# Performance work log

Measured on AMD Instinct MI355X. Metric: run time of the kernel, lower is better.

Reference implementation:

```python
import jax, jax.numpy as jnp
import numpy as np

B, E, H, L, V = 128, 1024, 1024, 2, 32001  # vocab = output_size + 1
PAD_IDX = 1000


def gru_cell(x, h, w_ih, w_hh, b_ih, b_hh):
    # PyTorch GRU cell math; gates ordered (r, z, n)
    gi = x @ w_ih.T + b_ih            # [B, 3H]
    gh = h @ w_hh.T + b_hh            # [B, 3H]
    i_r, i_z, i_n = jnp.split(gi, 3, axis=-1)
    h_r, h_z, h_n = jnp.split(gh, 3, axis=-1)
    r = jax.nn.sigmoid(i_r + h_r)
    z = jax.nn.sigmoid(i_z + h_z)
    n = jnp.tanh(i_n + r * h_n)
    return (1.0 - z) * n + z * h


def setup_inputs() -> dict:
    key = jax.random.key(0)
    ks = jax.random.split(key, 16)
    input_vector = jax.random.randint(ks[0], (B,), 0, V)
    hidden = jax.random.normal(ks[1], (L, B, H), dtype=jnp.float32)
    emb = jax.random.uniform(ks[2], (V, E), minval=-0.1, maxval=0.1, dtype=jnp.float32)
    emb = emb.at[PAD_IDX].set(0.0)  # padding_idx
    s = 1.0 / np.sqrt(H)
    def u(k, shape):
        return jax.random.uniform(k, shape, minval=-s, maxval=s, dtype=jnp.float32)
    w_ih0 = u(ks[3], (3 * H, E)); w_hh0 = u(ks[4], (3 * H, H))
    b_ih0 = u(ks[5], (3 * H,));  b_hh0 = u(ks[6], (3 * H,))
    w_ih1 = u(ks[7], (3 * H, H)); w_hh1 = u(ks[8], (3 * H, H))
    b_ih1 = u(ks[9], (3 * H,));  b_hh1 = u(ks[10], (3 * H,))
    w_out = jax.random.uniform(ks[11], (V, H), minval=-0.1, maxval=0.1, dtype=jnp.float32)
    b_out = jnp.zeros((V,), dtype=jnp.float32)
    return dict(input_vector=input_vector, hidden=hidden, emb=emb,
                w_ih0=w_ih0, w_hh0=w_hh0, b_ih0=b_ih0, b_hh0=b_hh0,
                w_ih1=w_ih1, w_hh1=w_hh1, b_ih1=b_ih1, b_hh1=b_hh1,
                w_out=w_out, b_out=b_out)


def reference(input_vector, hidden, emb, w_ih0, w_hh0, b_ih0, b_hh0,
              w_ih1, w_hh1, b_ih1, b_hh1, w_out, b_out):
    x = jax.nn.relu(emb[input_vector])          # [B, E] (seq_len=1 squeezed)
    h0 = gru_cell(x, hidden[0], w_ih0, w_hh0, b_ih0, b_hh0)   # [B, H]
    h1 = gru_cell(h0, hidden[1], w_ih1, w_hh1, b_ih1, b_hh1)  # [B, H]
    logits = h1 @ w_out.T + b_out               # [B, V]
    out = jax.nn.log_softmax(logits, axis=-1)   # [B, V]
    hidden_out = jnp.stack([h0, h1], axis=0)    # [L, B, H]
    return out, hidden_out
```

## Files before the change

### kernel.cpp

```cpp
#include <hip/hip_runtime.h>
#include <cmath>

#define BATCH 128
#define KDIM 1024
#define VOCAB 32001
#define G3 3072
#define GIP_STRIDE (BATCH * G3)

typedef __bf16 bf16_t;
typedef bf16_t bf16x8 __attribute__((ext_vector_type(8)));
typedef float f32x4 __attribute__((ext_vector_type(4)));

__device__ __forceinline__ void stage16(const void* g, void* lds) {
    __builtin_amdgcn_global_load_lds(
        (const __attribute__((address_space(1))) void*)g,
        (__attribute__((address_space(3))) void*)lds, 16, 0, 0);
}

template<bool BIAS>
__device__ __forceinline__ void gemm_core(
    const bf16_t* __restrict__ A, const float* __restrict__ W,
    const float* __restrict__ bias, float* __restrict__ C,
    int ldc, int Wrows, int n0, int kbeg, int kend)
{
    __shared__ bf16_t sA[128 * 64];
    __shared__ float  sB[64 * 64];
    const int t    = threadIdx.x;
    const int wave = t >> 6;
    const int lane = t & 63;
    const int l15  = lane & 15;
    const int quad = lane >> 4;
    const int wm   = wave & 1;
    const int wn   = wave >> 1;

    const bf16_t* aSrc[4]; int aDst[4];
#pragma unroll
    for (int r = 0; r < 4; ++r) {
        const int row = r * 32 + (t >> 3);
        const int sg  = t & 7;
        const int kg  = sg ^ (row & 7);
        aSrc[r] = A + (size_t)row * KDIM + kg * 8 + kbeg;
        aDst[r] = row * 128 + sg * 16;
    }
    const float* wSrc[4]; int wDst[4];
#pragma unroll
    for (int r = 0; r < 4; ++r) {
        const int row = r * 16 + (t >> 4);
        int wr = n0 + row; if (wr > Wrows - 1) wr = Wrows - 1;
        const int sg = t & 15;
        const int kg = sg ^ (row & 15);
        wSrc[r] = W + (size_t)wr * KDIM + kg * 4 + kbeg;
        wDst[r] = row * 256 + sg * 16;
    }

    f32x4 acc[4][2];
#pragma unroll
    for (int i = 0; i < 4; ++i)
#pragma unroll
        for (int j = 0; j < 2; ++j) acc[i][j] = f32x4{0.f, 0.f, 0.f, 0.f};

    for (int k0 = 0; k0 < kend - kbeg; k0 += 64) {
#pragma unroll
        for (int r = 0; r < 4; ++r) stage16(aSrc[r] + k0, (char*)sA + aDst[r]);
#pragma unroll
        for (int r = 0; r < 4; ++r) stage16(wSrc[r] + k0, (char*)sB + wDst[r]);
        __syncthreads();
#pragma unroll
        for (int s = 0; s < 2; ++s) {
            bf16x8 bfr[2];
#pragma unroll
            for (int j = 0; j < 2; ++j) {
                const int row = wn * 32 + j * 16 + l15;
                const int gu  = (s * 8 + 2 * quad) ^ (row & 15);
                const f32x4 u = *(const f32x4*)((const char*)sB + row * 256 + gu * 16);
                const f32x4 v = *(const f32x4*)((const char*)sB + row * 256 + (gu ^ 1) * 16);
                bf16x8 b;
                b[0] = (bf16_t)u[0]; b[1] = (bf16_t)u[1]; b[2] = (bf16_t)u[2]; b[3] = (bf16_t)u[3];
                b[4] = (bf16_t)v[0]; b[5] = (bf16_t)v[1]; b[6] = (bf16_t)v[2]; b[7] = (bf16_t)v[3];
                bfr[j] = b;
            }
#pragma unroll
            for (int i = 0; i < 4; ++i) {
                const int row  = wm * 64 + i * 16 + l15;
                const int phys = (s * 4 + quad) ^ (row & 7);
                const bf16x8 af = *(const bf16x8*)((const char*)sA + row * 128 + phys * 16);
#pragma unroll
                for (int j = 0; j < 2; ++j)
                    acc[i][j] = __builtin_amdgcn_mfma_f32_16x16x32_bf16(
                        af, bfr[j], acc[i][j], 0, 0, 0);
            }
        }
        __syncthreads();
    }

#pragma unroll
    for (int j = 0; j < 2; ++j) {
        const int col = n0 + wn * 32 + j * 16 + l15;
        if (col < Wrows) {
            const float bv = BIAS ? bias[col] : 0.f;
#pragma unroll
            for (int i = 0; i < 4; ++i)
#pragma unroll
                for (int r = 0; r < 4; ++r) {
                    const int row = wm * 64 + i * 16 + quad * 4 + r;
                    C[(size_t)row * ldc + col] = acc[i][j][r] + bv;
                }
        }
    }
}

__global__ __launch_bounds__(256, 4) void gemm_gru(
    const bf16_t* __restrict__ Ai, const float* __restrict__ wih,
    float* __restrict__ giP,
    const bf16_t* __restrict__ Ah, const float* __restrict__ whh,
    float* __restrict__ ghP)
{
    const int split = blockIdx.x;
    const int n0    = blockIdx.y * 64;
    const int kbeg  = split * 256;
    if (blockIdx.z == 0)
        gemm_core<false>(Ai, wih, nullptr, giP + (size_t)split * GIP_STRIDE,
                         G3, G3, n0, kbeg, kbeg + 256);
    else
        gemm_core<false>(Ah, whh, nullptr, ghP + (size_t)split * GIP_STRIDE,
                         G3, G3, n0, kbeg, kbeg + 256);
}

__global__ __launch_bounds__(256, 4) void gemm_vocab(
    const bf16_t* __restrict__ A, const float* __restrict__ W,
    const float* __restrict__ bias, float* __restrict__ C)
{
    gemm_core<true>(A, W, bias, C, VOCAB, VOCAB, blockIdx.x * 64, 0, KDIM);
}

__global__ __launch_bounds__(256) void prep_bf16(const int* __restrict__ idx,
                                                 const float* __restrict__ emb,
                                                 const float* __restrict__ hidden,
                                                 bf16_t* __restrict__ dst) {
    const int i = blockIdx.x * 256 + threadIdx.x;
    const int sec = i >> 15;
    const int j   = i & 32767;
    f32x4 v;
    if (sec == 0) {
        const int b = j >> 8, e4 = j & 255;
        v = ((const f32x4*)(emb + (size_t)idx[b] * KDIM))[e4];
#pragma unroll
        for (int k = 0; k < 4; ++k) v[k] = fmaxf(v[k], 0.f);
    } else {
        v = ((const f32x4*)(hidden + (size_t)(sec - 1) * (BATCH * KDIM)))[j];
    }
    bf16_t o[4];
#pragma unroll
    for (int k = 0; k < 4; ++k) o[k] = (bf16_t)v[k];
    *(uint64_t*)(dst + (size_t)i * 4) = *(const uint64_t*)o;
}

__device__ __forceinline__ f32x4 sum_splits(const float* p) {
    f32x4 s = *(const f32x4*)p;
    s += *(const f32x4*)(p + GIP_STRIDE);
    s += *(const f32x4*)(p + 2 * GIP_STRIDE);
    s += *(const f32x4*)(p + 3 * GIP_STRIDE);
    return s;
}

__global__ __launch_bounds__(256) void gru_gate(const float* __restrict__ giP,
                                                const float* __restrict__ ghP,
                                                const float* __restrict__ b_ih,
                                                const float* __restrict__ b_hh,
                                                const float* __restrict__ hprev,
                                                float* __restrict__ hout,
                                                bf16_t* __restrict__ hout_bf16) {
    const int i  = blockIdx.x * 256 + threadIdx.x;
    const int b  = i >> 8;
    const int j  = (i & 255) * 4;
    const size_t base = (size_t)b * G3 + j;

    f32x4 ir = sum_splits(giP + base),        hr = sum_splits(ghP + base);
    f32x4 iz = sum_splits(giP + base + 1024), hz = sum_splits(ghP + base + 1024);
    f32x4 in = sum_splits(giP + base + 2048), hn = sum_splits(ghP + base + 2048);
    const f32x4 bir = *(const f32x4*)(b_ih + j);
    const f32x4 biz = *(const f32x4*)(b_ih + j + 1024);
    const f32x4 bin = *(const f32x4*)(b_ih + j + 2048);
    const f32x4 bhr = *(const f32x4*)(b_hh + j);
    const f32x4 bhz = *(const f32x4*)(b_hh + j + 1024);
    const f32x4 bhn = *(const f32x4*)(b_hh + j + 2048);
    const f32x4 hp  = *(const f32x4*)(hprev + (size_t)b * KDIM + j);

    f32x4 o;
    bf16_t ob[4];
#pragma unroll
    for (int k = 0; k < 4; ++k) {
        const float r = 1.f / (1.f + __expf(-(ir[k] + bir[k] + hr[k] + bhr[k])));
        const float z = 1.f / (1.f + __expf(-(iz[k] + biz[k] + hz[k] + bhz[k])));
        const float a = in[k] + bin[k] + r * (hn[k] + bhn[k]);
        const float n = 1.f - 2.f / (__expf(2.f * a) + 1.f);
        o[k] = (1.f - z) * n + z * hp[k];
        ob[k] = (bf16_t)o[k];
    }
    *(f32x4*)(hout + (size_t)b * KDIM + j) = o;
    *(uint64_t*)(hout_bf16 + (size_t)b * KDIM + j) = *(const uint64_t*)ob;
}

__global__ __launch_bounds__(1024) void log_softmax_rows(float* __restrict__ out) {
    float* row = out + (size_t)blockIdx.x * VOCAB;
    const int t = threadIdx.x;
    __shared__ float sm[16], ss[16];

    float m = -3.4e38f, s = 0.f;
    for (int i = t; i < VOCAB; i += 1024) {
        const float v  = row[i];
        const float mn = fmaxf(m, v);
        s = s * __expf(m - mn) + __expf(v - mn);
        m = mn;
    }
#pragma unroll
    for (int o = 32; o; o >>= 1) {
        const float mo = __shfl_down(m, o);
        const float so = __shfl_down(s, o);
        const float mn = fmaxf(m, mo);
        s = s * __expf(m - mn) + so * __expf(mo - mn);
        m = mn;
    }
    if ((t & 63) == 0) { sm[t >> 6] = m; ss[t >> 6] = s; }
    __syncthreads();
    if (t == 0) {
        float M = sm[0], S = ss[0];
#pragma unroll
        for (int w = 1; w < 16; ++w) {
            const float mn = fmaxf(M, sm[w]);
            S = S * __expf(M - mn) + ss[w] * __expf(sm[w] - mn);
            M = mn;
        }
        sm[0] = M + __logf(S);
    }
    __syncthreads();
    const float L = sm[0];

    for (int i = t * 4; i + 3 < VOCAB; i += 4096) {
        f32x4 v = *(const f32x4*)(row + i);
        v[0] -= L; v[1] -= L; v[2] -= L; v[3] -= L;
        *(f32x4*)(row + i) = v;
    }
    if (t == 0) row[32000] -= L;
}

extern "C" void kernel_launch(void* const* d_in, const int* in_sizes, int n_in,
                              void* d_out, int out_size, void* d_ws, size_t ws_size,
                              hipStream_t stream) {
    const int*   ivec  = (const int*)  d_in[0];
    const float* hidden= (const float*)d_in[1];
    const float* emb   = (const float*)d_in[2];
    const float* w_ih0 = (const float*)d_in[3];
    const float* w_hh0 = (const float*)d_in[4];
    const float* b_ih0 = (const float*)d_in[5];
    const float* b_hh0 = (const float*)d_in[6];
    const float* w_ih1 = (const float*)d_in[7];
    const float* w_hh1 = (const float*)d_in[8];
    const float* b_ih1 = (const float*)d_in[9];
    const float* b_hh1 = (const float*)d_in[10];
    const float* w_out = (const float*)d_in[11];
    const float* b_out = (const float*)d_in[12];

    float* out = (float*)d_out;
    float* h0  = out + (size_t)BATCH * VOCAB;
    float* h1  = h0 + BATCH * KDIM;

    float*  ws   = (float*)d_ws;
    float*  giP  = ws;
    float*  ghP  = ws + 4 * (size_t)GIP_STRIDE;
    bf16_t* xb   = (bf16_t*)(ws + 8 * (size_t)GIP_STRIDE);
    bf16_t* hp0b = xb   + BATCH * KDIM;
    bf16_t* hp1b = hp0b + BATCH * KDIM;
    bf16_t* h0b  = hp1b + BATCH * KDIM;
    bf16_t* h1b  = h0b  + BATCH * KDIM;

    const float* hprev0 = hidden;
    const float* hprev1 = hidden + BATCH * KDIM;

    prep_bf16<<<384, 256, 0, stream>>>(ivec, emb, hidden, xb);

    gemm_gru<<<dim3(4, 48, 2), 256, 0, stream>>>(xb, w_ih0, giP, hp0b, w_hh0, ghP);
    gru_gate<<<128, 256, 0, stream>>>(giP, ghP, b_ih0, b_hh0, hprev0, h0, h0b);

    gemm_gru<<<dim3(4, 48, 2), 256, 0, stream>>>(h0b, w_ih1, giP, hp1b, w_hh1, ghP);
    gru_gate<<<128, 256, 0, stream>>>(giP, ghP, b_ih1, b_hh1, hprev1, h1, h1b);

    gemm_vocab<<<501, 256, 0, stream>>>(h1b, w_out, b_out, out);

    log_softmax_rows<<<128, 1024, 0, stream>>>(out);
}
```

Baseline: 336.6 us.

## Fuse softmax statistics into vocab GEMM epilogue and raise GRU split-K to 8

The vocab GEMM now computes per-row partial max/sum-exp for each 64-column tile in its epilogue and writes them to a stats buffer. A lighter softmax_final kernel merges those stats and subtracts the log-sum-exp over a 2D grid, so the extra full read pass over the logits goes away. The GRU GEMMs move from 4 to 8 K-splits for more parallelism, at the cost of more partial-sum traffic in the gate kernel. The vocab GEMM also doubles its K tile to 128 and drops to 2 blocks per CU, and the gate kernel now uses 128-thread blocks.

Result: no change. 338.0 us (+0.4%).

```diff
diff --git a/kernel.cpp b/kernel.cpp
--- a/kernel.cpp
+++ b/kernel.cpp
@@ -5,6 +5,7 @@
 #define KDIM 1024
 #define VOCAB 32001
 #define G3 3072
+#define NSPLIT 8
 #define GIP_STRIDE (BATCH * G3)
 
 typedef __bf16 bf16_t;
@@ -17,12 +18,25 @@
         (__attribute__((address_space(3))) void*)lds, 16, 0, 0);
 }
 
-template<bool BIAS>
-__device__ __forceinline__ void gemm_core(
-    const bf16_t* __restrict__ A, const float* __restrict__ W,
-    const float* __restrict__ bias, float* __restrict__ C,
-    int ldc, int Wrows, int n0, int kbeg, int kend)
+__device__ __forceinline__ void smerge(float& m, float& s, float mo, float so) {
+    const float mn = fmaxf(m, mo);
+    s = s * __expf(m - mn) + so * __expf(mo - mn);
+    m = mn;
+}
+
+__global__ __launch_bounds__(256, 4) void gemm_gru(
+    const bf16_t* __restrict__ Ai, const float* __restrict__ wih,
+    float* __restrict__ giP,
+    const bf16_t* __restrict__ Ah, const float* __restrict__ whh,
+    float* __restrict__ ghP)
 {
+    const int split = blockIdx.x;
+    const int n0    = blockIdx.y * 64;
+    const int kbeg  = split * 128;
+    const bf16_t* A; const float* W; float* C;
+    if (blockIdx.z == 0) { A = Ai; W = wih; C = giP + (size_t)split * GIP_STRIDE; }
+    else                 { A = Ah; W = whh; C = ghP + (size_t)split * GIP_STRIDE; }
+
     __shared__ bf16_t sA[128 * 64];
     __shared__ float  sB[64 * 64];
     const int t    = threadIdx.x;
@@ -38,18 +52,15 @@
     for (int r = 0; r < 4; ++r) {
         const int row = r * 32 + (t >> 3);
         const int sg  = t & 7;
-        const int kg  = sg ^ (row & 7);
-        aSrc[r] = A + (size_t)row * KDIM + kg * 8 + kbeg;
+        aSrc[r] = A + (size_t)row * KDIM + (sg ^ (row & 7)) * 8 + kbeg;
         aDst[r] = row * 128 + sg * 16;
     }
     const float* wSrc[4]; int wDst[4];
 #pragma unroll
     for (int r = 0; r < 4; ++r) {
         const int row = r * 16 + (t >> 4);
-        int wr = n0 + row; if (wr > Wrows - 1) wr = Wrows - 1;
-        const int sg = t & 15;
-        const int kg = sg ^ (row & 15);
-        wSrc[r] = W + (size_t)wr * KDIM + kg * 4 + kbeg;
+        const int sg  = t & 15;
+        wSrc[r] = W + (size_t)(n0 + row) * KDIM + (sg ^ (row & 15)) * 4 + kbeg;
         wDst[r] = row * 256 + sg * 16;
     }
 
@@ -59,7 +70,8 @@
 #pragma unroll
         for (int j = 0; j < 2; ++j) acc[i][j] = f32x4{0.f, 0.f, 0.f, 0.f};
 
-    for (int k0 = 0; k0 < kend - kbeg; k0 += 64) {
+#pragma unroll
+    for (int k0 = 0; k0 < 128; k0 += 64) {
 #pragma unroll
         for (int r = 0; r < 4; ++r) stage16(aSrc[r] + k0, (char*)sA + aDst[r]);
 #pragma unroll
@@ -96,41 +108,131 @@
 #pragma unroll
     for (int j = 0; j < 2; ++j) {
         const int col = n0 + wn * 32 + j * 16 + l15;
-        if (col < Wrows) {
-            const float bv = BIAS ? bias[col] : 0.f;
-#pragma unroll
-            for (int i = 0; i < 4; ++i)
-#pragma unroll
-                for (int r = 0; r < 4; ++r) {
-                    const int row = wm * 64 + i * 16 + quad * 4 + r;
-                    C[(size_t)row * ldc + col] = acc[i][j][r] + bv;
-                }
+#pragma unroll
+        for (int i = 0; i < 4; ++i)
+#pragma unroll
+            for (int r = 0; r < 4; ++r) {
+                const int row = wm * 64 + i * 16 + quad * 4 + r;
+                C[(size_t)row * G3 + col] = acc[i][j][r];
+            }
+    }
+}
+
+__global__ __launch_bounds__(256, 2) void gemm_vocab(
+    const bf16_t* __restrict__ A, const float* __restrict__ W,
+    const float* __restrict__ bias, float* __restrict__ C,
+    float2* __restrict__ stats)
+{
+    __shared__ bf16_t sA[128 * 128];
+    __shared__ float  sB[64 * 128];
+    const int t    = threadIdx.x;
+    const int wave = t >> 6;
+    const int lane = t & 63;
+    const int l15  = lane & 15;
+    const int quad = lane >> 4;
+    const int wm   = wave & 1;
+    const int wn   = wave >> 1;
+    const int n0   = blockIdx.x * 64;
+
+    const bf16_t* aSrc[8]; int aDst[8];
+#pragma unroll
+    for (int r = 0; r < 8; ++r) {
+        const int row = r * 16 + (t >> 4);
+        const int sg  = t & 15;
+        aSrc[r] = A + (size_t)row * KDIM + (sg ^ (row & 7)) * 8;
+        aDst[r] = row * 256 + sg * 16;
+    }
+    const float* wSrc[8]; int wDst[8];
+#pragma unroll
+    for (int r = 0; r < 8; ++r) {
+        const int row = r * 8 + (t >> 5);
+        int wr = n0 + row; if (wr > VOCAB - 1) wr = VOCAB - 1;
+        const int sg = t & 31;
+        wSrc[r] = W + (size_t)wr * KDIM + (sg ^ (row & 7)) * 4;
+        wDst[r] = row * 512 + sg * 16;
+    }
+
+    f32x4 acc[4][2];
+#pragma unroll
+    for (int i = 0; i < 4; ++i)
+#pragma unroll
+        for (int j = 0; j < 2; ++j) acc[i][j] = f32x4{0.f, 0.f, 0.f, 0.f};
+
+    for (int k0 = 0; k0 < KDIM; k0 += 128) {
+#pragma unroll
+        for (int r = 0; r < 8; ++r) stage16(aSrc[r] + k0, (char*)sA + aDst[r]);
+#pragma unroll
+        for (int r = 0; r < 8; ++r) stage16(wSrc[r] + k0, (char*)sB + wDst[r]);
+        __syncthreads();
+#pragma unroll
+        for (int s = 0; s < 4; ++s) {
+            bf16x8 bfr[2];
+#pragma unroll
+            for (int j = 0; j < 2; ++j) {
+                const int row = wn * 32 + j * 16 + l15;
+                const int g0  = s * 8 + quad * 2;
+                const int p0  = g0 ^ (row & 7);
+                const int p1  = (g0 + 1) ^ (row & 7);
+                const f32x4 u = *(const f32x4*)((const char*)sB + row * 512 + p0 * 16);
+                const f32x4 v = *(const f32x4*)((const char*)sB + row * 512 + p1 * 16);
+                bf16x8 b;
+                b[0] = (bf16_t)u[0]; b[1] = (bf16_t)u[1]; b[2] = (bf16_t)u[2]; b[3] = (bf16_t)u[3];
+                b[4] = (bf16_t)v[0]; b[5] = (bf16_t)v[1]; b[6] = (bf16_t)v[2]; b[7] = (bf16_t)v[3];
+                bfr[j] = b;
+            }
+#pragma unroll
+            for (int i = 0; i < 4; ++i) {
+                const int row  = wm * 64 + i * 16 + l15;
+                const int phys = (s * 4 + quad) ^ (row & 7);
+                const bf16x8 af = *(const bf16x8*)((const char*)sA + row * 256 + phys * 16);
+#pragma unroll
+                for (int j = 0; j < 2; ++j)
+                    acc[i][j] = __builtin_amdgcn_mfma_f32_16x16x32_bf16(
+                        af, bfr[j], acc[i][j], 0, 0, 0);
+            }
         }
-    }
-}
-
-__global__ __launch_bounds__(256, 4) void gemm_gru(
-    const bf16_t* __restrict__ Ai, const float* __restrict__ wih,
-    float* __restrict__ giP,
-    const bf16_t* __restrict__ Ah, const float* __restrict__ whh,
-    float* __restrict__ ghP)
-{
-    const int split = blockIdx.x;
-    const int n0    = blockIdx.y * 64;
-    const int kbeg  = split * 256;
-    if (blockIdx.z == 0)
-        gemm_core<false>(Ai, wih, nullptr, giP + (size_t)split * GIP_STRIDE,
-                         G3, G3, n0, kbeg, kbeg + 256);
-    else
-        gemm_core<false>(Ah, whh, nullptr, ghP + (size_t)split * GIP_STRIDE,
-                         G3, G3, n0, kbeg, kbeg + 256);
-}
-
-__global__ __launch_bounds__(256, 4) void gemm_vocab(
-    const bf16_t* __restrict__ A, const float* __restrict__ W,
-    const float* __restrict__ bias, float* __restrict__ C)
-{
-    gemm_core<true>(A, W, bias, C, VOCAB, VOCAB, blockIdx.x * 64, 0, KDIM);
+        __syncthreads();
+    }
+
+    int   col[2]; float bv[2];
+#pragma unroll
+    for (int j = 0; j < 2; ++j) {
+        col[j] = n0 + wn * 32 + j * 16 + l15;
+        bv[j]  = (col[j] < VOCAB) ? bias[col[j]] : 0.f;
+    }
+    float rm[4][4], rs[4][4];
+#pragma unroll
+    for (int i = 0; i < 4; ++i)
+#pragma unroll
+        for (int r = 0; r < 4; ++r) {
+            const int grow = wm * 64 + i * 16 + quad * 4 + r;
+            float v0 = acc[i][0][r] + bv[0];
+            float v1 = acc[i][1][r] + bv[1];
+            if (col[0] < VOCAB) C[(size_t)grow * VOCAB + col[0]] = v0; else v0 = -3.4e38f;
+            if (col[1] < VOCAB) C[(size_t)grow * VOCAB + col[1]] = v1; else v1 = -3.4e38f;
+            const float mm = fmaxf(v0, v1);
+            rm[i][r] = mm;
+            rs[i][r] = __expf(v0 - mm) + __expf(v1 - mm);
+#pragma unroll
+            for (int o = 1; o < 16; o <<= 1)
+                smerge(rm[i][r], rs[i][r], __shfl_xor(rm[i][r], o), __shfl_xor(rs[i][r], o));
+        }
+
+    __syncthreads();
+    float2* sst = (float2*)sA;
+#pragma unroll
+    for (int i = 0; i < 4; ++i)
+#pragma unroll
+        for (int r = 0; r < 4; ++r)
+            if (l15 == 0)
+                sst[wn * 128 + wm * 64 + i * 16 + quad * 4 + r] =
+                    make_float2(rm[i][r], rs[i][r]);
+    __syncthreads();
+    if (t < 128) {
+        float2 a = sst[t], b = sst[128 + t];
+        smerge(a.x, a.y, b.x, b.y);
+        stats[(size_t)t * 512 + blockIdx.x] = a;
+    }
 }
 
 __global__ __launch_bounds__(256) void prep_bf16(const int* __restrict__ idx,
@@ -157,20 +259,19 @@
 
 __device__ __forceinline__ f32x4 sum_splits(const float* p) {
     f32x4 s = *(const f32x4*)p;
-    s += *(const f32x4*)(p + GIP_STRIDE);
-    s += *(const f32x4*)(p + 2 * GIP_STRIDE);
-    s += *(const f32x4*)(p + 3 * GIP_STRIDE);
+#pragma unroll
+    for (int k = 1; k < NSPLIT; ++k) s += *(const f32x4*)(p + (size_t)k * GIP_STRIDE);
     return s;
 }
 
-__global__ __launch_bounds__(256) void gru_gate(const float* __restrict__ giP,
+__global__ __launch_bounds__(128) void gru_gate(const float* __restrict__ giP,
                                                 const float* __restrict__ ghP,
                                                 const float* __restrict__ b_ih,
                                                 const float* __restrict__ b_hh,
                                                 const float* __restrict__ hprev,
                                                 float* __restrict__ hout,
                                                 bf16_t* __restrict__ hout_bf16) {
-    const int i  = blockIdx.x * 256 + threadIdx.x;
+    const int i  = blockIdx.x * 128 + threadIdx.x;
     const int b  = i >> 8;
     const int j  = (i & 255) * 4;
     const size_t base = (size_t)b * G3 + j;
@@ -201,47 +302,40 @@
     *(uint64_t*)(hout_bf16 + (size_t)b * KDIM + j) = *(const uint64_t*)ob;
 }
 
-__global__ __launch_bounds__(1024) void log_softmax_rows(float* __restrict__ out) {
-    float* row = out + (size_t)blockIdx.x * VOCAB;
-    const int t = threadIdx.x;
-    __shared__ float sm[16], ss[16];
-
+__global__ __launch_bounds__(256) void softmax_final(float* __restrict__ out,
+                                                     const float2* __restrict__ stats) {
+    const int row = blockIdx.x, chunk = blockIdx.y, t = threadIdx.x;
     float m = -3.4e38f, s = 0.f;
-    for (int i = t; i < VOCAB; i += 1024) {
-        const float v  = row[i];
-        const float mn = fmaxf(m, v);
-        s = s * __expf(m - mn) + __expf(v - mn);
-        m = mn;
+    for (int k = t; k < 501; k += 256) {
+        const float2 p = stats[(size_t)row * 512 + k];
+        smerge(m, s, p.x, p.y);
     }
 #pragma unroll
     for (int o = 32; o; o >>= 1) {
         const float mo = __shfl_down(m, o);
         const float so = __shfl_down(s, o);
-        const float mn = fmaxf(m, mo);
-        s = s * __expf(m - mn) + so * __expf(mo - mn);
-        m = mn;
-    }
-    if ((t & 63) == 0) { sm[t >> 6] = m; ss[t >> 6] = s; }
+        smerge(m, s, mo, so);
+    }
+    __shared__ float sm[4], ssu[4], sL;
+    if ((t & 63) == 0) { sm[t >> 6] = m; ssu[t >> 6] = s; }
     __syncthreads();
     if (t == 0) {
-        float M = sm[0], S = ss[0];
-#pragma unroll
-        for (int w = 1; w < 16; ++w) {
-            const float mn = fmaxf(M, sm[w]);
-            S = S * __expf(M - mn) + ss[w] * __expf(sm[w] - mn);
-            M = mn;
-        }
-        sm[0] = M + __logf(S);
+        float M = sm[0], S = ssu[0];
+#pragma unroll
+        for (int w = 1; w < 4; ++w) smerge(M, S, sm[w], ssu[w]);
+        sL = M + __logf(S);
     }
     __syncthreads();
-    const float L = sm[0];
-
-    for (int i = t * 4; i + 3 < VOCAB; i += 4096) {
-        f32x4 v = *(const f32x4*)(row + i);
+    const float L = sL;
+
+    float* rowp = out + (size_t)row * VOCAB;
+    const int g = chunk * 256 + t;
+    for (int i = g * 4; i + 3 < VOCAB; i += 4096) {
+        f32x4 v = *(const f32x4*)(rowp + i);
         v[0] -= L; v[1] -= L; v[2] -= L; v[3] -= L;
-        *(f32x4*)(row + i) = v;
-    }
-    if (t == 0) row[32000] -= L;
+        *(f32x4*)(rowp + i) = v;
+    }
+    if (g == 0) rowp[32000] -= L;
 }
 
 extern "C" void kernel_launch(void* const* d_in, const int* in_sizes, int n_in,
@@ -265,27 +359,28 @@
     float* h0  = out + (size_t)BATCH * VOCAB;
     float* h1  = h0 + BATCH * KDIM;
 
-    float*  ws   = (float*)d_ws;
-    float*  giP  = ws;
-    float*  ghP  = ws + 4 * (size_t)GIP_STRIDE;
-    bf16_t* xb   = (bf16_t*)(ws + 8 * (size_t)GIP_STRIDE);
-    bf16_t* hp0b = xb   + BATCH * KDIM;
-    bf16_t* hp1b = hp0b + BATCH * KDIM;
-    bf16_t* h0b  = hp1b + BATCH * KDIM;
-    bf16_t* h1b  = h0b  + BATCH * KDIM;
+    float*  ws    = (float*)d_ws;
+    float*  giP   = ws;
+    float*  ghP   = ws + (size_t)NSPLIT * GIP_STRIDE;
+    bf16_t* xb    = (bf16_t*)(ws + 2 * (size_t)NSPLIT * GIP_STRIDE);
+    bf16_t* hp0b  = xb   + BATCH * KDIM;
+    bf16_t* hp1b  = hp0b + BATCH * KDIM;
+    bf16_t* h0b   = hp1b + BATCH * KDIM;
+    bf16_t* h1b   = h0b  + BATCH * KDIM;
+    float2* stats = (float2*)(h1b + BATCH * KDIM);
 
     const float* hprev0 = hidden;
     const float* hprev1 = hidden + BATCH * KDIM;
 
     prep_bf16<<<384, 256, 0, stream>>>(ivec, emb, hidden, xb);
 
-    gemm_gru<<<dim3(4, 48, 2), 256, 0, stream>>>(xb, w_ih0, giP, hp0b, w_hh0, ghP);
-    gru_gate<<<128, 256, 0, stream>>>(giP, ghP, b_ih0, b_hh0, hprev0, h0, h0b);
-
-    gemm_gru<<<dim3(4, 48, 2), 256, 0, stream>>>(h0b, w_ih1, giP, hp1b, w_hh1, ghP);
-    gru_gate<<<128, 256, 0, stream>>>(giP, ghP, b_ih1, b_hh1, hprev1, h1, h1b);
-
-    gemm_vocab<<<501, 256, 0, stream>>>(h1b, w_out, b_out, out);
-
-    log_softmax_rows<<<128, 1024, 0, stream>>>(out);
-}
+    gemm_gru<<<dim3(8, 48, 2), 256, 0, stream>>>(xb, w_ih0, giP, hp0b, w_hh0, ghP);
+    gru_gate<<<256, 128, 0, stream>>>(giP, ghP, b_ih0, b_hh0, hprev0, h0, h0b);
+
+    gemm_gru<<<dim3(8, 48, 2), 256, 0, stream>>>(h0b, w_ih1, giP, hp1b, w_hh1, ghP);
+    gru_gate<<<256, 128, 0, stream>>>(giP, ghP, b_ih1, b_hh1, hprev1, h1, h1b);
+
+    gemm_vocab<<<501, 256, 0, stream>>>(h1b, w_out, b_out, out, stats);
+
+    softmax_final<<<dim3(128, 4), 256, 0, stream>>>(out, stats);
+}
```
